# Kernel optimization log

Measured on AMD Instinct MI355X. Metric: run time of the kernel, lower is better.

Reference implementation:

```python
import jax, jax.numpy as jnp
import numpy as np

B = 32          # decode batch (one query token per sequence)
HID = 4096      # hidden_size
H = 32          # num_heads
D = 128         # head_dim
BLK = 16        # KV-cache block size (vLLM default)
MAXB = 64       # max blocks per sequence
NBLK = 2048     # total cache blocks
S = MAXB * BLK  # max context length = 1024
ROPE_THETA = 10000.0


def _rope(x, positions):
    # x: [B, H, D], positions: [B] int. GPT-NeoX / Llama half-split rotary.
    half = D // 2
    inv_freq = 1.0 / (ROPE_THETA ** (jnp.arange(0, half, dtype=jnp.float32) / half))
    freqs = positions.astype(jnp.float32)[:, None] * inv_freq[None, :]  # [B, D/2]
    cos = jnp.cos(freqs)[:, None, :]  # [B, 1, D/2]
    sin = jnp.sin(freqs)[:, None, :]
    x1, x2 = x[..., :half], x[..., half:]
    return jnp.concatenate([x1 * cos - x2 * sin, x1 * sin + x2 * cos], axis=-1)


def setup_inputs() -> dict:
    key = jax.random.key(0)
    ks = jax.random.split(key, 8)
    hidden_states = jax.random.normal(ks[0], (B, HID), jnp.float32)
    Wq = jax.random.normal(ks[1], (HID, HID), jnp.float32) * 0.02
    Wk = jax.random.normal(ks[2], (HID, HID), jnp.float32) * 0.02
    Wv = jax.random.normal(ks[3], (HID, HID), jnp.float32) * 0.02
    Wo = jax.random.normal(ks[4], (HID, HID), jnp.float32) * 0.02
    k_cache = jax.random.normal(ks[5], (NBLK, BLK, H, D), jnp.float32)
    v_cache = jax.random.normal(ks[6], (NBLK, BLK, H, D), jnp.float32)
    # each sequence owns MAXB distinct cache blocks (non-contiguous)
    block_tables = jax.random.permutation(ks[7], NBLK)[: B * MAXB].reshape(B, MAXB).astype(jnp.int32)
    context_lens = jax.random.randint(jax.random.fold_in(key, 9), (B,), S // 2, S + 1).astype(jnp.int32)
    positions = context_lens - 1  # current token position
    slot_mapping = (block_tables[jnp.arange(B), positions // BLK] * BLK + positions % BLK).astype(jnp.int32)
    return dict(hidden_states=hidden_states, k_cache=k_cache, v_cache=v_cache,
                Wq=Wq, Wk=Wk, Wv=Wv, Wo=Wo,
                positions=positions, slot_mapping=slot_mapping,
                block_tables=block_tables, context_lens=context_lens)


def reference(hidden_states, k_cache, v_cache, Wq, Wk, Wv, Wo,
              positions, slot_mapping, block_tables, context_lens):
    # QKV projections (bias-free, torch Linear convention: x @ W.T)
    q = (hidden_states @ Wq.T).reshape(B, H, D)
    k = (hidden_states @ Wk.T).reshape(B, H, D)
    v = (hidden_states @ Wv.T).reshape(B, H, D)
    q = _rope(q, positions)
    k = _rope(k, positions)
    # write new k/v into the paged cache at slot_mapping
    kc = k_cache.reshape(NBLK * BLK, H, D).at[slot_mapping].set(k)
    vc = v_cache.reshape(NBLK * BLK, H, D).at[slot_mapping].set(v)
    kc = kc.reshape(NBLK, BLK, H, D)
    vc = vc.reshape(NBLK, BLK, H, D)
    # paged gather: [B, MAXB, BLK, H, D] -> [B, S, H, D]
    keys = kc[block_tables].reshape(B, S, H, D)
    vals = vc[block_tables].reshape(B, S, H, D)
    scores = jnp.einsum('bhd,bshd->bhs', q, keys) * (D ** -0.5)
    valid = jnp.arange(S)[None, :] < context_lens[:, None]  # [B, S]
    scores = jnp.where(valid[:, None, :], scores, jnp.float32(-1e30))
    probs = jax.nn.softmax(scores, axis=-1)
    attn = jnp.einsum('bhs,bshd->bhd', probs, vals).reshape(B, H * D)
    return attn @ Wo.T
```

## Files before the change

kernel.cpp:

```cpp
#include <hip/hip_runtime.h>
#include <math.h>

#define HID 4096
#define B 32
#define H 32
#define D 128
#define KBLK 16
#define MAXB 64
#define CHUNK 256
#define NCHUNK 4

template <int MODE>
__global__ __launch_bounds__(256) void gemv_kernel(
    const float* __restrict__ W0, const float* __restrict__ W1, const float* __restrict__ W2,
    const float* __restrict__ x, const int* __restrict__ positions, float* __restrict__ out)
{
    __shared__ float wt[8][256];
    __shared__ float buf[4][8][66];
    const int bid = blockIdx.x;
    const int mat = (MODE == 0) ? (bid >> 9) : 0;
    const int sub = bid & 511;
    const bool rope = (MODE == 0) && (mat < 2);
    const int head = sub >> 4;
    const int p0 = (sub & 15) << 2;
    const float* W = (mat == 0) ? W0 : ((mat == 1) ? W1 : W2);
    float* outp = out + (size_t)mat * (B * HID);

    const int tid = threadIdx.x;
    const int lane = tid & 63;
    const int wid = tid >> 6;
    const int b0 = wid << 3;

    float acc[8][8];
#pragma unroll
    for (int c = 0; c < 8; ++c)
#pragma unroll
        for (int j = 0; j < 8; ++j) acc[c][j] = 0.f;

    for (int k0 = 0; k0 < HID; k0 += 256) {
        __syncthreads();
#pragma unroll
        for (int i = 0; i < 2; ++i) {
            int idx = tid + (i << 8);
            int r = idx >> 6;
            int c4 = idx & 63;
            int cr = rope ? (head * 128 + p0 + (r & 3) + ((r >> 2) << 6))
                          : ((sub << 3) + r);
            float4 v = *reinterpret_cast<const float4*>(
                &W[(size_t)cr * HID + k0 + (c4 << 2)]);
            *reinterpret_cast<float4*>(&wt[r][c4 << 2]) = v;
        }
        __syncthreads();

        float4 hs4[8];
#pragma unroll
        for (int j = 0; j < 8; ++j)
            hs4[j] = *reinterpret_cast<const float4*>(
                &x[(size_t)(b0 + j) * HID + k0 + (lane << 2)]);

#pragma unroll
        for (int c = 0; c < 8; ++c) {
            float4 w4 = *reinterpret_cast<const float4*>(&wt[c][lane << 2]);
#pragma unroll
            for (int j = 0; j < 8; ++j) {
                acc[c][j] += w4.x * hs4[j].x;
                acc[c][j] += w4.y * hs4[j].y;
                acc[c][j] += w4.z * hs4[j].z;
                acc[c][j] += w4.w * hs4[j].w;
            }
        }
    }

    float res[8];
#pragma unroll
    for (int c = 0; c < 8; ++c) {
#pragma unroll
        for (int j = 0; j < 8; ++j) buf[wid][j][lane] = acc[c][j];
        __builtin_amdgcn_sched_barrier(0);
        const float* rp = &buf[wid][lane >> 3][(lane & 7) << 3];
        float4 a = *reinterpret_cast<const float4*>(rp);
        float4 bb = *reinterpret_cast<const float4*>(rp + 4);
        __builtin_amdgcn_sched_barrier(0);
        float s = ((a.x + a.y) + (a.z + a.w)) + ((bb.x + bb.y) + (bb.z + bb.w));
        s += __shfl_xor(s, 1, 64);
        s += __shfl_xor(s, 2, 64);
        s += __shfl_xor(s, 4, 64);
        res[c] = s;
    }

    const int jme = lane >> 3;
    const int cme = lane & 7;
    float myv;
    if (rope) {
        const float pf = (float)positions[b0 + jme];
        float ro[8];
#pragma unroll
        for (int cc = 0; cc < 4; ++cc) {
            float invf = exp2f(-(float)(p0 + cc) * 0.20762050593046013f);
            float f = pf * invf;
            float cs = cosf(f), sn = sinf(f);
            ro[cc]     = res[cc] * cs - res[cc + 4] * sn;
            ro[cc + 4] = res[cc] * sn + res[cc + 4] * cs;
        }
        myv = ro[0];
#pragma unroll
        for (int cc = 1; cc < 8; ++cc) myv = (cme == cc) ? ro[cc] : myv;
    } else {
        myv = res[0];
#pragma unroll
        for (int cc = 1; cc < 8; ++cc) myv = (cme == cc) ? res[cc] : myv;
    }
    const int colw = rope ? (head * 128 + p0 + (cme & 3) + ((cme >> 2) << 6))
                          : ((sub << 3) + cme);
    outp[(size_t)(b0 + jme) * HID + colw] = myv;
}

__global__ __launch_bounds__(256) void attn_partial_kernel(
    const float* __restrict__ qkv,
    const float* __restrict__ k_cache,
    const float* __restrict__ v_cache,
    const int* __restrict__ block_tables,
    const int* __restrict__ context_lens,
    const int* __restrict__ positions,
    float* __restrict__ pm,
    float* __restrict__ pl,
    float* __restrict__ po)
{
    const int h = blockIdx.x;
    const int c = blockIdx.y;
    const int b = blockIdx.z;
    const int L = context_lens[b];
    const int s0 = c << 8;
    if (s0 >= L) return;
    const int Lc = min(L - s0, CHUNK);
    const int pos = positions[b];
    const int tid = threadIdx.x;

    __shared__ float sc[CHUNK];
    __shared__ float red[8];
    __shared__ int btl[16];
    __shared__ float o4[4][D];

    if (tid < 16) btl[tid] = block_tables[b * MAXB + (c << 4) + tid];
    __syncthreads();

    const float* qptr = qkv + (size_t)b * HID + h * D;
    const float* knew = qkv + (size_t)(B * HID) + (size_t)b * HID + h * D;
    const float* vnew = qkv + (size_t)(2 * B * HID) + (size_t)b * HID + h * D;
    const float scale = 0.088388347648318447f;

    const int hw = tid >> 5;
    const int hl = tid & 31;
    const float4 qv = *reinterpret_cast<const float4*>(qptr + (hl << 2));

    int i = hw;
    for (; i + 24 < Lc; i += 32) {
        const int sA = s0 + i, sB = sA + 8, sC = sA + 16, sD = sA + 24;
        const float* kp0 = (sA == pos) ? knew
            : k_cache + ((size_t)(btl[i >> 4] * KBLK + (sA & 15)) * H + h) * D;
        const float* kp1 = (sB == pos) ? knew
            : k_cache + ((size_t)(btl[(i + 8) >> 4] * KBLK + (sB & 15)) * H + h) * D;
        const float* kp2 = (sC == pos) ? knew
            : k_cache + ((size_t)(btl[(i + 16) >> 4] * KBLK + (sC & 15)) * H + h) * D;
        const float* kp3 = (sD == pos) ? knew
            : k_cache + ((size_t)(btl[(i + 24) >> 4] * KBLK + (sD & 15)) * H + h) * D;
        float4 k0 = *reinterpret_cast<const float4*>(kp0 + (hl << 2));
        float4 k1 = *reinterpret_cast<const float4*>(kp1 + (hl << 2));
        float4 k2 = *reinterpret_cast<const float4*>(kp2 + (hl << 2));
        float4 k3 = *reinterpret_cast<const float4*>(kp3 + (hl << 2));
        float d0 = qv.x * k0.x + qv.y * k0.y + qv.z * k0.z + qv.w * k0.w;
        float d1 = qv.x * k1.x + qv.y * k1.y + qv.z * k1.z + qv.w * k1.w;
        float d2 = qv.x * k2.x + qv.y * k2.y + qv.z * k2.z + qv.w * k2.w;
        float d3 = qv.x * k3.x + qv.y * k3.y + qv.z * k3.z + qv.w * k3.w;
#pragma unroll
        for (int m = 16; m; m >>= 1) {
            d0 += __shfl_xor(d0, m, 64);
            d1 += __shfl_xor(d1, m, 64);
            d2 += __shfl_xor(d2, m, 64);
            d3 += __shfl_xor(d3, m, 64);
        }
        if (hl == 0) {
            sc[i] = d0 * scale; sc[i + 8] = d1 * scale;
            sc[i + 16] = d2 * scale; sc[i + 24] = d3 * scale;
        }
    }
    for (; i < Lc; i += 8) {
        const int sA = s0 + i;
        const float* kp = (sA == pos) ? knew
            : k_cache + ((size_t)(btl[i >> 4] * KBLK + (sA & 15)) * H + h) * D;
        float4 k0 = *reinterpret_cast<const float4*>(kp + (hl << 2));
        float d0 = qv.x * k0.x + qv.y * k0.y + qv.z * k0.z + qv.w * k0.w;
#pragma unroll
        for (int m = 16; m; m >>= 1) d0 += __shfl_xor(d0, m, 64);
        if (hl == 0) sc[i] = d0 * scale;
    }
    for (; i < CHUNK; i += 8)
        if (hl == 0) sc[i] = -1e30f;
    __syncthreads();

    const int w = tid >> 6;
    const float xv = sc[tid];
    float m = xv;
#pragma unroll
    for (int mm = 32; mm; mm >>= 1) m = fmaxf(m, __shfl_xor(m, mm, 64));
    if ((tid & 63) == 0) red[w] = m;
    __syncthreads();
    const float gm = fmaxf(fmaxf(red[0], red[1]), fmaxf(red[2], red[3]));

    float p = (xv > -1e29f) ? __expf(xv - gm) : 0.f;
    sc[tid] = p;
    float l = p;
#pragma unroll
    for (int mm = 32; mm; mm >>= 1) l += __shfl_xor(l, mm, 64);
    if ((tid & 63) == 0) red[4 + w] = l;
    __syncthreads();
    const float gl = red[4] + red[5] + red[6] + red[7];

    const int l2 = (tid & 63) << 1;
    float accx = 0.f, accy = 0.f;
    i = w;
    for (; i + 12 < Lc; i += 16) {
        const int sA = s0 + i, sB = sA + 4, sC = sA + 8, sD = sA + 12;
        const float* vp0 = (sA == pos) ? vnew
            : v_cache + ((size_t)(btl[i >> 4] * KBLK + (sA & 15)) * H + h) * D;
        const float* vp1 = (sB == pos) ? vnew
            : v_cache + ((size_t)(btl[(i + 4) >> 4] * KBLK + (sB & 15)) * H + h) * D;
        const float* vp2 = (sC == pos) ? vnew
            : v_cache + ((size_t)(btl[(i + 8) >> 4] * KBLK + (sC & 15)) * H + h) * D;
        const float* vp3 = (sD == pos) ? vnew
            : v_cache + ((size_t)(btl[(i + 12) >> 4] * KBLK + (sD & 15)) * H + h) * D;
        float2 v0 = *reinterpret_cast<const float2*>(vp0 + l2);
        float2 v1 = *reinterpret_cast<const float2*>(vp1 + l2);
        float2 v2 = *reinterpret_cast<const float2*>(vp2 + l2);
        float2 v3 = *reinterpret_cast<const float2*>(vp3 + l2);
        float p0 = sc[i], p1 = sc[i + 4], p2 = sc[i + 8], p3 = sc[i + 12];
        accx += p0 * v0.x; accy += p0 * v0.y;
        accx += p1 * v1.x; accy += p1 * v1.y;
        accx += p2 * v2.x; accy += p2 * v2.y;
        accx += p3 * v3.x; accy += p3 * v3.y;
    }
    for (; i < Lc; i += 4) {
        const float* vp = (s0 + i == pos) ? vnew
            : v_cache + ((size_t)(btl[i >> 4] * KBLK + ((s0 + i) & 15)) * H + h) * D;
        float2 v0 = *reinterpret_cast<const float2*>(vp + l2);
        float p0 = sc[i];
        accx += p0 * v0.x; accy += p0 * v0.y;
    }
    o4[w][l2] = accx;
    o4[w][l2 + 1] = accy;
    __syncthreads();

    const int bh = b * H + h;
    if (tid < D) {
        float o = o4[0][tid] + o4[1][tid] + o4[2][tid] + o4[3][tid];
        po[((size_t)bh * NCHUNK + c) * D + tid] = o;
    } else if (tid == D) {
        pm[bh * NCHUNK + c] = gm;
        pl[bh * NCHUNK + c] = gl;
    }
}

__global__ __launch_bounds__(128) void attn_combine_kernel(
    const float* __restrict__ pm, const float* __restrict__ pl,
    const float* __restrict__ po, const int* __restrict__ context_lens,
    float* __restrict__ attn_out)
{
    const int bh = blockIdx.x;
    const int b = bh >> 5;
    const int tid = threadIdx.x;
    const int nc = (context_lens[b] + CHUNK - 1) >> 8;

    float m = -1e30f;
    for (int c = 0; c < nc; ++c) m = fmaxf(m, pm[bh * NCHUNK + c]);
    float wsum = 0.f, o = 0.f;
    for (int c = 0; c < nc; ++c) {
        float wc = __expf(pm[bh * NCHUNK + c] - m);
        wsum += wc * pl[bh * NCHUNK + c];
        o += wc * po[((size_t)bh * NCHUNK + c) * D + tid];
    }
    attn_out[(size_t)bh * D + tid] = o / wsum;
}

extern "C" void kernel_launch(void* const* d_in, const int* in_sizes, int n_in,
                              void* d_out, int out_size, void* d_ws, size_t ws_size,
                              hipStream_t stream) {
    const float* hs        = (const float*)d_in[0];
    const float* k_cache   = (const float*)d_in[1];
    const float* v_cache   = (const float*)d_in[2];
    const float* Wq        = (const float*)d_in[3];
    const float* Wk        = (const float*)d_in[4];
    const float* Wv        = (const float*)d_in[5];
    const float* Wo        = (const float*)d_in[6];
    const int*   positions = (const int*)d_in[7];
    const int*   block_tables = (const int*)d_in[9];
    const int*   context_lens = (const int*)d_in[10];
    float* out = (float*)d_out;

    float* qkv     = (float*)d_ws;
    float* attn_ws = qkv + (size_t)3 * B * HID;
    float* pm      = attn_ws + (size_t)B * HID;
    float* pl      = pm + (size_t)B * H * NCHUNK;
    float* po      = pl + (size_t)B * H * NCHUNK;

    gemv_kernel<0><<<dim3(3 * 512), 256, 0, stream>>>(Wq, Wk, Wv, hs, positions, qkv);
    attn_partial_kernel<<<dim3(H, NCHUNK, B), 256, 0, stream>>>(
        qkv, k_cache, v_cache, block_tables, context_lens, positions, pm, pl, po);
    attn_combine_kernel<<<dim3(B * H), 128, 0, stream>>>(pm, pl, po, context_lens, attn_ws);
    gemv_kernel<1><<<dim3(512), 256, 0, stream>>>(Wo, Wo, Wo, attn_ws, positions, out);
}
```

Measured before the change: 262.5 us.

## Process all heads per token row in attention partial kernel

```diff
diff --git a/kernel.cpp b/kernel.cpp
--- a/kernel.cpp
+++ b/kernel.cpp
@@ -7,8 +7,8 @@
 #define D 128
 #define KBLK 16
 #define MAXB 64
-#define CHUNK 256
-#define NCHUNK 4
+#define CH 128
+#define NCH 8
 
 template <int MODE>
 __global__ __launch_bounds__(256) void gemv_kernel(
@@ -126,138 +126,142 @@
     float* __restrict__ pl,
     float* __restrict__ po)
 {
-    const int h = blockIdx.x;
-    const int c = blockIdx.y;
-    const int b = blockIdx.z;
+    const int c = blockIdx.x;
+    const int b = blockIdx.y;
     const int L = context_lens[b];
-    const int s0 = c << 8;
+    const int s0 = c << 7;
     if (s0 >= L) return;
-    const int Lc = min(L - s0, CHUNK);
+    const int Lc = min(L - s0, CH);
     const int pos = positions[b];
-    const int tid = threadIdx.x;
-
-    __shared__ float sc[CHUNK];
-    __shared__ float red[8];
-    __shared__ int btl[16];
-    __shared__ float o4[4][D];
-
-    if (tid < 16) btl[tid] = block_tables[b * MAXB + (c << 4) + tid];
+    const int t = threadIdx.x;
+
+    __shared__ float ps[32][CH + 1];
+    __shared__ float mred[32], lred[32];
+    __shared__ int btl[8];
+    if (t < 8) btl[t] = block_tables[b * MAXB + (c << 3) + t];
     __syncthreads();
 
-    const float* qptr = qkv + (size_t)b * HID + h * D;
-    const float* knew = qkv + (size_t)(B * HID) + (size_t)b * HID + h * D;
-    const float* vnew = qkv + (size_t)(2 * B * HID) + (size_t)b * HID + h * D;
+    const float* qb   = qkv + (size_t)b * HID;
+    const float* knew = qkv + (size_t)(B * HID) + (size_t)b * HID;
+    const float* vnew = qkv + (size_t)(2 * B * HID) + (size_t)b * HID;
     const float scale = 0.088388347648318447f;
 
-    const int hw = tid >> 5;
-    const int hl = tid & 31;
-    const float4 qv = *reinterpret_cast<const float4*>(qptr + (hl << 2));
-
-    int i = hw;
-    for (; i + 24 < Lc; i += 32) {
-        const int sA = s0 + i, sB = sA + 8, sC = sA + 16, sD = sA + 24;
-        const float* kp0 = (sA == pos) ? knew
-            : k_cache + ((size_t)(btl[i >> 4] * KBLK + (sA & 15)) * H + h) * D;
-        const float* kp1 = (sB == pos) ? knew
-            : k_cache + ((size_t)(btl[(i + 8) >> 4] * KBLK + (sB & 15)) * H + h) * D;
-        const float* kp2 = (sC == pos) ? knew
-            : k_cache + ((size_t)(btl[(i + 16) >> 4] * KBLK + (sC & 15)) * H + h) * D;
-        const float* kp3 = (sD == pos) ? knew
-            : k_cache + ((size_t)(btl[(i + 24) >> 4] * KBLK + (sD & 15)) * H + h) * D;
-        float4 k0 = *reinterpret_cast<const float4*>(kp0 + (hl << 2));
-        float4 k1 = *reinterpret_cast<const float4*>(kp1 + (hl << 2));
-        float4 k2 = *reinterpret_cast<const float4*>(kp2 + (hl << 2));
-        float4 k3 = *reinterpret_cast<const float4*>(kp3 + (hl << 2));
-        float d0 = qv.x * k0.x + qv.y * k0.y + qv.z * k0.z + qv.w * k0.w;
-        float d1 = qv.x * k1.x + qv.y * k1.y + qv.z * k1.z + qv.w * k1.w;
-        float d2 = qv.x * k2.x + qv.y * k2.y + qv.z * k2.z + qv.w * k2.w;
-        float d3 = qv.x * k3.x + qv.y * k3.y + qv.z * k3.z + qv.w * k3.w;
-#pragma unroll
-        for (int m = 16; m; m >>= 1) {
-            d0 += __shfl_xor(d0, m, 64);
-            d1 += __shfl_xor(d1, m, 64);
-            d2 += __shfl_xor(d2, m, 64);
-            d3 += __shfl_xor(d3, m, 64);
-        }
-        if (hl == 0) {
-            sc[i] = d0 * scale; sc[i + 8] = d1 * scale;
-            sc[i + 16] = d2 * scale; sc[i + 24] = d3 * scale;
-        }
-    }
-    for (; i < Lc; i += 8) {
-        const int sA = s0 + i;
-        const float* kp = (sA == pos) ? knew
-            : k_cache + ((size_t)(btl[i >> 4] * KBLK + (sA & 15)) * H + h) * D;
-        float4 k0 = *reinterpret_cast<const float4*>(kp + (hl << 2));
-        float d0 = qv.x * k0.x + qv.y * k0.y + qv.z * k0.z + qv.w * k0.w;
-#pragma unroll
-        for (int m = 16; m; m >>= 1) d0 += __shfl_xor(d0, m, 64);
-        if (hl == 0) sc[i] = d0 * scale;
-    }
-    for (; i < CHUNK; i += 8)
-        if (hl == 0) sc[i] = -1e30f;
+    const int hsub = t >> 5;
+    const int hl5  = t & 31;
+
+    const float4 q0 = *reinterpret_cast<const float4*>(qb + ((0 * 256 + t) << 2));
+    const float4 q1 = *reinterpret_cast<const float4*>(qb + ((1 * 256 + t) << 2));
+    const float4 q2 = *reinterpret_cast<const float4*>(qb + ((2 * 256 + t) << 2));
+    const float4 q3 = *reinterpret_cast<const float4*>(qb + ((3 * 256 + t) << 2));
+
+#define QK_BODY(s)                                                                 \
+    {                                                                              \
+        const int gs = s0 + (s);                                                   \
+        const float* kb = (gs == pos) ? knew                                       \
+            : k_cache + (size_t)(btl[(s) >> 4] * KBLK + (gs & 15)) * (H * D);      \
+        float4 k0 = *reinterpret_cast<const float4*>(kb + ((0 * 256 + t) << 2));   \
+        float4 k1 = *reinterpret_cast<const float4*>(kb + ((1 * 256 + t) << 2));   \
+        float4 k2 = *reinterpret_cast<const float4*>(kb + ((2 * 256 + t) << 2));   \
+        float4 k3 = *reinterpret_cast<const float4*>(kb + ((3 * 256 + t) << 2));   \
+        float d0 = q0.x * k0.x + q0.y * k0.y + q0.z * k0.z + q0.w * k0.w;          \
+        float d1 = q1.x * k1.x + q1.y * k1.y + q1.z * k1.z + q1.w * k1.w;          \
+        float d2 = q2.x * k2.x + q2.y * k2.y + q2.z * k2.z + q2.w * k2.w;          \
+        float d3 = q3.x * k3.x + q3.y * k3.y + q3.z * k3.z + q3.w * k3.w;          \
+        _Pragma("unroll")                                                          \
+        for (int m = 1; m <= 16; m <<= 1) {                                        \
+            d0 += __shfl_xor(d0, m, 64);                                           \
+            d1 += __shfl_xor(d1, m, 64);                                           \
+            d2 += __shfl_xor(d2, m, 64);                                           \
+            d3 += __shfl_xor(d3, m, 64);                                           \
+        }                                                                          \
+        if (hl5 == 0) {                                                            \
+            ps[hsub][s]      = d0 * scale;                                         \
+            ps[8 + hsub][s]  = d1 * scale;                                         \
+            ps[16 + hsub][s] = d2 * scale;                                         \
+            ps[24 + hsub][s] = d3 * scale;                                         \
+        }                                                                          \
+    }
+
+    {
+        int s = 0;
+        for (; s + 1 < Lc; s += 2) {
+            QK_BODY(s);
+            QK_BODY(s + 1);
+        }
+        if (s < Lc) QK_BODY(s);
+    }
     __syncthreads();
 
-    const int w = tid >> 6;
-    const float xv = sc[tid];
-    float m = xv;
-#pragma unroll
-    for (int mm = 32; mm; mm >>= 1) m = fmaxf(m, __shfl_xor(m, mm, 64));
-    if ((tid & 63) == 0) red[w] = m;
+    const int hh = t >> 3;
+    const int so = t & 7;
+    float m = -1e30f;
+#pragma unroll
+    for (int k = 0; k < 16; ++k) {
+        int s = so + (k << 3);
+        if (s < Lc) m = fmaxf(m, ps[hh][s]);
+    }
+    m = fmaxf(m, __shfl_xor(m, 1, 64));
+    m = fmaxf(m, __shfl_xor(m, 2, 64));
+    m = fmaxf(m, __shfl_xor(m, 4, 64));
+    if (so == 0) mred[hh] = m;
     __syncthreads();
-    const float gm = fmaxf(fmaxf(red[0], red[1]), fmaxf(red[2], red[3]));
-
-    float p = (xv > -1e29f) ? __expf(xv - gm) : 0.f;
-    sc[tid] = p;
-    float l = p;
-#pragma unroll
-    for (int mm = 32; mm; mm >>= 1) l += __shfl_xor(l, mm, 64);
-    if ((tid & 63) == 0) red[4 + w] = l;
+    const float gm = mred[hh];
+    float l = 0.f;
+#pragma unroll
+    for (int k = 0; k < 16; ++k) {
+        int s = so + (k << 3);
+        if (s < Lc) {
+            float pv = __expf(ps[hh][s] - gm);
+            ps[hh][s] = pv;
+            l += pv;
+        }
+    }
+    l += __shfl_xor(l, 1, 64);
+    l += __shfl_xor(l, 2, 64);
+    l += __shfl_xor(l, 4, 64);
+    if (so == 0) lred[hh] = l;
     __syncthreads();
-    const float gl = red[4] + red[5] + red[6] + red[7];
-
-    const int l2 = (tid & 63) << 1;
-    float accx = 0.f, accy = 0.f;
-    i = w;
-    for (; i + 12 < Lc; i += 16) {
-        const int sA = s0 + i, sB = sA + 4, sC = sA + 8, sD = sA + 12;
-        const float* vp0 = (sA == pos) ? vnew
-            : v_cache + ((size_t)(btl[i >> 4] * KBLK + (sA & 15)) * H + h) * D;
-        const float* vp1 = (sB == pos) ? vnew
-            : v_cache + ((size_t)(btl[(i + 4) >> 4] * KBLK + (sB & 15)) * H + h) * D;
-        const float* vp2 = (sC == pos) ? vnew
-            : v_cache + ((size_t)(btl[(i + 8) >> 4] * KBLK + (sC & 15)) * H + h) * D;
-        const float* vp3 = (sD == pos) ? vnew
-            : v_cache + ((size_t)(btl[(i + 12) >> 4] * KBLK + (sD & 15)) * H + h) * D;
-        float2 v0 = *reinterpret_cast<const float2*>(vp0 + l2);
-        float2 v1 = *reinterpret_cast<const float2*>(vp1 + l2);
-        float2 v2 = *reinterpret_cast<const float2*>(vp2 + l2);
-        float2 v3 = *reinterpret_cast<const float2*>(vp3 + l2);
-        float p0 = sc[i], p1 = sc[i + 4], p2 = sc[i + 8], p3 = sc[i + 12];
-        accx += p0 * v0.x; accy += p0 * v0.y;
-        accx += p1 * v1.x; accy += p1 * v1.y;
-        accx += p2 * v2.x; accy += p2 * v2.y;
-        accx += p3 * v3.x; accy += p3 * v3.y;
-    }
-    for (; i < Lc; i += 4) {
-        const float* vp = (s0 + i == pos) ? vnew
-            : v_cache + ((size_t)(btl[i >> 4] * KBLK + ((s0 + i) & 15)) * H + h) * D;
-        float2 v0 = *reinterpret_cast<const float2*>(vp + l2);
-        float p0 = sc[i];
-        accx += p0 * v0.x; accy += p0 * v0.y;
-    }
-    o4[w][l2] = accx;
-    o4[w][l2 + 1] = accy;
-    __syncthreads();
-
-    const int bh = b * H + h;
-    if (tid < D) {
-        float o = o4[0][tid] + o4[1][tid] + o4[2][tid] + o4[3][tid];
-        po[((size_t)bh * NCHUNK + c) * D + tid] = o;
-    } else if (tid == D) {
-        pm[bh * NCHUNK + c] = gm;
-        pl[bh * NCHUNK + c] = gl;
-    }
+
+    float4 o0 = {0.f, 0.f, 0.f, 0.f}, o1 = o0, o2 = o0, o3 = o0;
+
+#define PV_BODY(s)                                                                 \
+    {                                                                              \
+        const int gs = s0 + (s);                                                   \
+        const float* vb = (gs == pos) ? vnew                                       \
+            : v_cache + (size_t)(btl[(s) >> 4] * KBLK + (gs & 15)) * (H * D);      \
+        float4 v0 = *reinterpret_cast<const float4*>(vb + ((0 * 256 + t) << 2));   \
+        float4 v1 = *reinterpret_cast<const float4*>(vb + ((1 * 256 + t) << 2));   \
+        float4 v2 = *reinterpret_cast<const float4*>(vb + ((2 * 256 + t) << 2));   \
+        float4 v3 = *reinterpret_cast<const float4*>(vb + ((3 * 256 + t) << 2));   \
+        float pA = ps[hsub][s], pB = ps[8 + hsub][s];                              \
+        float pC = ps[16 + hsub][s], pD = ps[24 + hsub][s];                        \
+        o0.x += pA * v0.x; o0.y += pA * v0.y; o0.z += pA * v0.z; o0.w += pA * v0.w;\
+        o1.x += pB * v1.x; o1.y += pB * v1.y; o1.z += pB * v1.z; o1.w += pB * v1.w;\
+        o2.x += pC * v2.x; o2.y += pC * v2.y; o2.z += pC * v2.z; o2.w += pC * v2.w;\
+        o3.x += pD * v3.x; o3.y += pD * v3.y; o3.z += pD * v3.z; o3.w += pD * v3.w;\
+    }
+
+    {
+        int s = 0;
+        for (; s + 1 < Lc; s += 2) {
+            PV_BODY(s);
+            PV_BODY(s + 1);
+        }
+        if (s < Lc) PV_BODY(s);
+    }
+
+    const int dd = hl5 << 2;
+    const size_t bh = (size_t)b * H;
+    *reinterpret_cast<float4*>(&po[((bh + hsub)      * NCH + c) * D + dd]) = o0;
+    *reinterpret_cast<float4*>(&po[((bh + 8 + hsub)  * NCH + c) * D + dd]) = o1;
+    *reinterpret_cast<float4*>(&po[((bh + 16 + hsub) * NCH + c) * D + dd]) = o2;
+    *reinterpret_cast<float4*>(&po[((bh + 24 + hsub) * NCH + c) * D + dd]) = o3;
+    if (t < 32) {
+        pm[(bh + t) * NCH + c] = mred[t];
+        pl[(bh + t) * NCH + c] = lred[t];
+    }
+#undef QK_BODY
+#undef PV_BODY
 }
 
 __global__ __launch_bounds__(128) void attn_combine_kernel(
@@ -268,15 +272,15 @@
     const int bh = blockIdx.x;
     const int b = bh >> 5;
     const int tid = threadIdx.x;
-    const int nc = (context_lens[b] + CHUNK - 1) >> 8;
+    const int nc = (context_lens[b] + CH - 1) >> 7;
 
     float m = -1e30f;
-    for (int c = 0; c < nc; ++c) m = fmaxf(m, pm[bh * NCHUNK + c]);
+    for (int c = 0; c < nc; ++c) m = fmaxf(m, pm[bh * NCH + c]);
     float wsum = 0.f, o = 0.f;
     for (int c = 0; c < nc; ++c) {
-        float wc = __expf(pm[bh * NCHUNK + c] - m);
-        wsum += wc * pl[bh * NCHUNK + c];
-        o += wc * po[((size_t)bh * NCHUNK + c) * D + tid];
+        float wc = __expf(pm[bh * NCH + c] - m);
+        wsum += wc * pl[bh * NCH + c];
+        o += wc * po[((size_t)bh * NCH + c) * D + tid];
     }
     attn_out[(size_t)bh * D + tid] = o / wsum;
 }
@@ -299,11 +303,11 @@
     float* qkv     = (float*)d_ws;
     float* attn_ws = qkv + (size_t)3 * B * HID;
     float* pm      = attn_ws + (size_t)B * HID;
-    float* pl      = pm + (size_t)B * H * NCHUNK;
-    float* po      = pl + (size_t)B * H * NCHUNK;
+    float* pl      = pm + (size_t)B * H * NCH;
+    float* po      = pl + (size_t)B * H * NCH;
 
     gemv_kernel<0><<<dim3(3 * 512), 256, 0, stream>>>(Wq, Wk, Wv, hs, positions, qkv);
-    attn_partial_kernel<<<dim3(H, NCHUNK, B), 256, 0, stream>>>(
+    attn_partial_kernel<<<dim3(NCH, B), 256, 0, stream>>>(
         qkv, k_cache, v_cache, block_tables, context_lens, positions, pm, pl, po);
     attn_combine_kernel<<<dim3(B * H), 128, 0, stream>>>(pm, pl, po, context_lens, attn_ws);
     gemv_kernel<1><<<dim3(512), 256, 0, stream>>>(Wo, Wo, Wo, attn_ws, positions, out);
```

Measured after the change: 387.5 us. 47.7% more time.
